# Kernel tuning notes

Measured on AMD Instinct MI355X. Metric: run time of the kernel, lower is better.

Reference implementation:

```python
import jax, jax.numpy as jnp
import numpy as np
from jax import lax

EPS = 1e-8

def setup_inputs() -> dict:
    key = jax.random.key(0)
    k1, k2, k3, k4 = jax.random.split(key, 4)
    b, ic, oc, ks, sd, h, w = 16, 512, 512, 3, 512, 64, 64
    x = jax.random.normal(k1, (b, ic, h, w), dtype=jnp.float32)
    style = jax.random.normal(k2, (b, sd), dtype=jnp.float32)
    # kaiming_normal_(fan_in, linear): std = 1/sqrt(ic*ks*ks)
    weight = jax.random.normal(k3, (oc, ic, ks, ks), dtype=jnp.float32) / np.sqrt(ic * ks * ks)
    bias = jnp.zeros((oc,), dtype=jnp.float32)
    # nn.Linear default init ~ U(-1/sqrt(sd), 1/sqrt(sd)); normal approx is fine for a baseline
    mod_w = jax.random.normal(k4, (ic, sd), dtype=jnp.float32) / np.sqrt(sd)
    mod_b = jnp.ones((ic,), dtype=jnp.float32)  # bias initialized to 1.0 in the module
    return {"x": x, "style": style, "weight": weight, "bias": bias, "mod_w": mod_w, "mod_b": mod_b}

def reference(x, style, weight, bias, mod_w, mod_b):
    b, ic, h, w = x.shape
    oc, _, ks, _ = weight.shape
    # style modulation: [b, ic]
    s = style @ mod_w.T + mod_b
    # per-sample modulated weights: [b, oc, ic, k, k]
    wmod = weight[None] * s[:, None, :, None, None]
    # demodulation
    demod = lax.rsqrt(jnp.sum(wmod * wmod, axis=(2, 3, 4)) + EPS)  # [b, oc]
    wmod = wmod * demod[:, :, None, None, None]
    pad = ks // 2
    # grouped conv with groups=b == per-sample conv: vmap over batch
    def conv1(xi, wi):  # xi: [ic,h,w], wi: [oc,ic,k,k]
        return lax.conv_general_dilated(
            xi[None], wi, window_strides=(1, 1),
            padding=[(pad, pad), (pad, pad)],
            dimension_numbers=("NCHW", "OIHW", "NCHW"))[0]
    out = jax.vmap(conv1)(x, wmod)  # [b, oc, h, w]
    return out + bias[None, :, None, None]
```

## Files before the change

### kernel.cpp

```cpp
#include <hip/hip_runtime.h>
#include <hip/hip_bf16.h>


typedef __bf16 bf16x8 __attribute__((ext_vector_type(8)));
typedef float  f32x4  __attribute__((ext_vector_type(4)));

#define IC   512
#define OC   512
#define HW   4096
#define KTOT 4608

typedef __attribute__((address_space(3))) unsigned lds_u32;
typedef const __attribute__((address_space(1))) unsigned glb_u32;
#define GLL16(gsrc, ldst) \
    __builtin_amdgcn_global_load_lds((glb_u32*)(gsrc), (lds_u32*)(ldst), 16, 0, 0)
#define VMW(N) asm volatile("s_waitcnt vmcnt(" #N ")" ::: "memory")
#define BAR()  asm volatile("s_barrier" ::: "memory")

__global__ __launch_bounds__(256) void style_mod_kernel(
    const float* __restrict__ style, const float* __restrict__ mod_w,
    const float* __restrict__ mod_b, float* __restrict__ s_out)
{
    int pair = blockIdx.x * 4 + (threadIdx.x >> 6);
    int lane = threadIdx.x & 63;
    int b = pair >> 9;
    int i = pair & 511;
    const float4* sv = (const float4*)(style + b * 512);
    const float4* wv = (const float4*)(mod_w + i * 512);
    float4 a0 = sv[lane * 2], a1 = sv[lane * 2 + 1];
    float4 w0 = wv[lane * 2], w1 = wv[lane * 2 + 1];
    float sum = a0.x*w0.x + a0.y*w0.y + a0.z*w0.z + a0.w*w0.w
              + a1.x*w1.x + a1.y*w1.y + a1.z*w1.z + a1.w*w1.w;
    #pragma unroll
    for (int off = 32; off; off >>= 1) sum += __shfl_xor(sum, off);
    if (lane == 0) s_out[pair] = sum + mod_b[i];
}

__global__ __launch_bounds__(256) void wmod_kernel(
    const float* __restrict__ weight,
    const float* __restrict__ s_in,
    __hip_bfloat16* __restrict__ wmod)
{
    int b  = blockIdx.x >> 9;
    int oc = blockIdx.x & 511;
    __shared__ float s_sh[512];
    __shared__ float red[256];
    int t = threadIdx.x;
    s_sh[t]       = s_in[b * 512 + t];
    s_sh[t + 256] = s_in[b * 512 + t + 256];
    __syncthreads();
    const float* wrow = weight + (size_t)oc * KTOT;
    float partial = 0.f;
    for (int e = t; e < KTOT; e += 256) {
        float v = wrow[e] * s_sh[e / 9];
        partial += v * v;
    }
    red[t] = partial;
    __syncthreads();
    #pragma unroll
    for (int off = 128; off; off >>= 1) {
        if (t < off) red[t] += red[t + off];
        __syncthreads();
    }
    float demod = rsqrtf(red[0] + 1e-8f);
    __hip_bfloat16* dst = wmod + (size_t)blockIdx.x * KTOT;
    for (int ep = t; ep < KTOT; ep += 256) {
        int tap = ep >> 9, ic = ep & 511;
        dst[ep] = __float2bfloat16(wrow[ic * 9 + tap] * s_sh[ic] * demod);
    }
}

__global__ void zero_row_kernel(__hip_bfloat16* xT) {
    ((unsigned*)(xT + ((size_t)blockIdx.x * 4097 + 4096) * 512))[threadIdx.x] = 0u;
}

__global__ __launch_bounds__(256) void xpose_kernel(
    const float* __restrict__ x, __hip_bfloat16* __restrict__ xT)
{
    __shared__ __align__(16) float tile[64][68];
    int b = blockIdx.z, ic0 = blockIdx.y * 64, p0 = blockIdx.x * 64;
    int t = threadIdx.x;
    const float* xb = x + ((size_t)b * 512 + ic0) * 4096 + p0;
    int rr = t >> 4, cc = (t & 15) * 4;
    #pragma unroll
    for (int i = 0; i < 4; ++i) {
        float4 v = *(const float4*)(xb + (size_t)(rr + i * 16) * 4096 + cc);
        *(float4*)&tile[rr + i * 16][cc] = v;
    }
    __syncthreads();
    int pr = t >> 2, io = (t & 3) * 16;
    __hip_bfloat16 obuf[16];
    #pragma unroll
    for (int j = 0; j < 16; ++j) obuf[j] = __float2bfloat16(tile[io + j][pr]);
    __hip_bfloat16* dst = xT + ((size_t)b * 4097 + p0 + pr) * 512 + ic0 + io;
    *(uint4*)dst       = *(uint4*)&obuf[0];
    *(uint4*)(dst + 8) = *(uint4*)&obuf[8];
}

__global__ __launch_bounds__(512, 2) void conv_kernel(
    const __hip_bfloat16* __restrict__ xT,
    const __hip_bfloat16* __restrict__ wmod,
    const float* __restrict__ bias,
    float* __restrict__ out)
{
    __shared__ __align__(16) __hip_bfloat16 Ash[4][256 * 32];
    __shared__ __align__(16) __hip_bfloat16 Bsh[4][256 * 32];

    const int t    = threadIdx.x;
    const int lane = t & 63;
    const int wid  = t >> 6;
    const int wm   = wid >> 2;
    const int wn   = wid & 3;
    const int lr   = lane & 15;
    const int lq   = lane >> 4;

    int bid = blockIdx.x;
    int xcd = bid & 7, idx = bid >> 3;
    int oc1 = idx & 1;
    int nt  = (idx >> 1) & 15;
    int bb  = (idx >> 5) & 1;
    int b   = xcd * 2 + bb;
    int oc0 = oc1 * 256, n0 = nt * 256;

    const __hip_bfloat16* wb = wmod + (size_t)(b * 512 + oc0) * KTOT;
    const __hip_bfloat16* xb = xT + (size_t)b * 4097 * 512;

    const int qoff = (((t & 3) ^ ((t >> 3) & 3)) * 8);
    const int srow = t >> 2;
    const int p0g  = n0 + srow;
    const int y0p  = p0g >> 6, x0p = p0g & 63;

    const __hip_bfloat16* pA0 = wb + (size_t)srow * KTOT + qoff;
    const __hip_bfloat16* pA1 = pA0 + (size_t)128 * KTOT;

    const int swq = (lq ^ ((lr >> 1) & 3)) * 8;
    const int arb = (wm * 128 + lr) * 32 + swq;
    const int brb = (wn * 64  + lr) * 32 + swq;

    f32x4 acc[8][4] = {};

    auto bptrs = [&](int tap, const __hip_bfloat16*& P0, const __hip_bfloat16*& P1) {
        int dy = tap / 3 - 1, dx = tap % 3 - 1;
        int sy = y0p + dy, sx = x0p + dx;
        int pix0 = ((((unsigned)sy)  < 64u) & (((unsigned)sx) < 64u)) ? ((sy  << 6) + sx) : 4096;
        int sy1 = sy + 2;
        int pix1 = ((((unsigned)sy1) < 64u) & (((unsigned)sx) < 64u)) ? ((sy1 << 6) + sx) : 4096;
        P0 = xb + (size_t)pix0 * 512 + qoff;
        P1 = xb + (size_t)pix1 * 512 + qoff;
    };

#define STAGE(SB, PA_OFF, Q0, Q1, B_OFF) { \
    GLL16(pA0 + (PA_OFF), &Ash[SB][t * 8]); \
    GLL16(pA1 + (PA_OFF), &Ash[SB][(t + 512) * 8]); \
    GLL16((Q0) + (B_OFF), &Bsh[SB][t * 8]); \
    GLL16((Q1) + (B_OFF), &Bsh[SB][(t + 512) * 8]); }

#define COMPUTE(CB) { \
    bf16x8 af[8], bf[4]; \
    _Pragma("unroll") for (int mi = 0; mi < 8; ++mi) \
        af[mi] = *(const bf16x8*)(&Ash[CB][arb + mi * 512]); \
    _Pragma("unroll") for (int ni = 0; ni < 4; ++ni) \
        bf[ni] = *(const bf16x8*)(&Bsh[CB][brb + ni * 512]); \
    __builtin_amdgcn_s_setprio(1); \
    _Pragma("unroll") for (int mi = 0; mi < 8; ++mi) \
        _Pragma("unroll") for (int ni = 0; ni < 4; ++ni) \
            acc[mi][ni] = __builtin_amdgcn_mfma_f32_16x16x32_bf16( \
                af[mi], bf[ni], acc[mi][ni], 0, 0, 0); \
    __builtin_amdgcn_s_setprio(0); }

    const __hip_bfloat16 *pB0, *pB1, *nB0, *nB1;
    bptrs(0, pB0, pB1);

    STAGE(0, 0,  pB0, pB1, 0);
    STAGE(1, 32, pB0, pB1, 32);
    STAGE(2, 64, pB0, pB1, 64);
    VMW(8);
    BAR();

    for (int tap = 0; tap < 8; ++tap) {
        bptrs(tap + 1, nB0, nB1);
        #pragma unroll
        for (int ch = 0; ch < 16; ++ch) {
            if (ch < 13) { STAGE((ch + 3) & 3, (ch + 3) * 32, pB0, pB1, (ch + 3) * 32); }
            else         { STAGE((ch + 3) & 3, (ch + 3) * 32, nB0, nB1, (ch - 13) * 32); }
            COMPUTE(ch & 3);
            VMW(8);
            BAR();
        }
        pA0 += 512; pA1 += 512;
        pB0 = nB0; pB1 = nB1;
    }
    #pragma unroll
    for (int ch = 0; ch < 16; ++ch) {
        if (ch <= 12) { STAGE((ch + 3) & 3, (ch + 3) * 32, pB0, pB1, (ch + 3) * 32); }
        COMPUTE(ch & 3);
        if      (ch < 13)  { VMW(8); BAR(); }
        else if (ch == 13) { VMW(4); BAR(); }
        else if (ch == 14) { VMW(0); BAR(); }
    }
#undef STAGE
#undef COMPUTE

    #pragma unroll
    for (int mi = 0; mi < 8; ++mi) {
        int oc = oc0 + wm * 128 + mi * 16 + lq * 4;
        #pragma unroll
        for (int ni = 0; ni < 4; ++ni) {
            int n = n0 + wn * 64 + ni * 16 + lr;
            #pragma unroll
            for (int v = 0; v < 4; ++v) {
                float r = acc[mi][ni][v] + bias[oc + v];
                out[((size_t)(b * OC + oc + v)) * HW + n] = r;
            }
        }
    }
}

extern "C" void kernel_launch(void* const* d_in, const int* in_sizes, int n_in,
                              void* d_out, int out_size, void* d_ws, size_t ws_size,
                              hipStream_t stream) {
    const float* x      = (const float*)d_in[0];
    const float* style  = (const float*)d_in[1];
    const float* weight = (const float*)d_in[2];
    const float* bias   = (const float*)d_in[3];
    const float* mod_w  = (const float*)d_in[4];
    const float* mod_b  = (const float*)d_in[5];
    float* out = (float*)d_out;

    float* s_ws = (float*)d_ws;
    __hip_bfloat16* wmod = (__hip_bfloat16*)((char*)d_ws + 32768);
    __hip_bfloat16* xT   = (__hip_bfloat16*)((char*)d_ws + 32768 + (size_t)16 * 512 * KTOT * 2);

    style_mod_kernel<<<2048, 256, 0, stream>>>(style, mod_w, mod_b, s_ws);
    wmod_kernel<<<16 * 512, 256, 0, stream>>>(weight, s_ws, wmod);
    zero_row_kernel<<<16, 256, 0, stream>>>(xT);
    dim3 tgrid(64, 8, 16);
    xpose_kernel<<<tgrid, 256, 0, stream>>>(x, xT);
    conv_kernel<<<512, 512, 0, stream>>>(xT, wmod, bias, out);
}
```

Before: 379.4 us.

## Split conv K-chunk into two MFMA halves interleaved with staged loads and barriers

Each K-chunk of the conv main loop is now split into two halves. The A fragments for rows 0-3 and the B fragments are read, the A global-to-LDS load is issued, then 16 MFMAs run; then A rows 4-7 are read, the B load is issued, and another 16 MFMAs run. Extra s_barriers and sched_barrier(0) fences pin this ordering so LDS reads, async global loads and MFMA phases overlap across waves, in a ping-pong style schedule. The change halves the live A-fragment registers, but it adds two barriers per chunk and constrains the compiler's scheduling freedom.

```diff
diff --git a/kernel.cpp b/kernel.cpp
--- a/kernel.cpp
+++ b/kernel.cpp
@@ -14,8 +14,9 @@
 typedef const __attribute__((address_space(1))) unsigned glb_u32;
 #define GLL16(gsrc, ldst) \
     __builtin_amdgcn_global_load_lds((glb_u32*)(gsrc), (lds_u32*)(ldst), 16, 0, 0)
-#define VMW(N) asm volatile("s_waitcnt vmcnt(" #N ")" ::: "memory")
-#define BAR()  asm volatile("s_barrier" ::: "memory")
+#define VMW(N)  asm volatile("s_waitcnt vmcnt(" #N ")" ::: "memory")
+#define BAR()   asm volatile("s_barrier" ::: "memory")
+#define SCHED0() __builtin_amdgcn_sched_barrier(0)
 
 __global__ __launch_bounds__(256) void style_mod_kernel(
     const float* __restrict__ style, const float* __restrict__ mod_w,
@@ -149,31 +150,27 @@
         P1 = xb + (size_t)pix1 * 512 + qoff;
     };
 
-#define STAGE(SB, PA_OFF, Q0, Q1, B_OFF) { \
-    GLL16(pA0 + (PA_OFF), &Ash[SB][t * 8]); \
-    GLL16(pA1 + (PA_OFF), &Ash[SB][(t + 512) * 8]); \
-    GLL16((Q0) + (B_OFF), &Bsh[SB][t * 8]); \
-    GLL16((Q1) + (B_OFF), &Bsh[SB][(t + 512) * 8]); }
-
-#define COMPUTE(CB) { \
-    bf16x8 af[8], bf[4]; \
-    _Pragma("unroll") for (int mi = 0; mi < 8; ++mi) \
-        af[mi] = *(const bf16x8*)(&Ash[CB][arb + mi * 512]); \
-    _Pragma("unroll") for (int ni = 0; ni < 4; ++ni) \
-        bf[ni] = *(const bf16x8*)(&Bsh[CB][brb + ni * 512]); \
+#define STAGE_A(SB, OFF) { \
+    GLL16(pA0 + (OFF), &Ash[SB][t * 8]); \
+    GLL16(pA1 + (OFF), &Ash[SB][(t + 512) * 8]); }
+#define STAGE_B(SB, Q0, Q1, OFF) { \
+    GLL16((Q0) + (OFF), &Bsh[SB][t * 8]); \
+    GLL16((Q1) + (OFF), &Bsh[SB][(t + 512) * 8]); }
+
+#define MFMA_HALF(MB) { \
     __builtin_amdgcn_s_setprio(1); \
-    _Pragma("unroll") for (int mi = 0; mi < 8; ++mi) \
+    _Pragma("unroll") for (int mi = 0; mi < 4; ++mi) \
         _Pragma("unroll") for (int ni = 0; ni < 4; ++ni) \
-            acc[mi][ni] = __builtin_amdgcn_mfma_f32_16x16x32_bf16( \
-                af[mi], bf[ni], acc[mi][ni], 0, 0, 0); \
+            acc[(MB) + mi][ni] = __builtin_amdgcn_mfma_f32_16x16x32_bf16( \
+                af[mi], bfr[ni], acc[(MB) + mi][ni], 0, 0, 0); \
     __builtin_amdgcn_s_setprio(0); }
 
     const __hip_bfloat16 *pB0, *pB1, *nB0, *nB1;
     bptrs(0, pB0, pB1);
 
-    STAGE(0, 0,  pB0, pB1, 0);
-    STAGE(1, 32, pB0, pB1, 32);
-    STAGE(2, 64, pB0, pB1, 64);
+    STAGE_A(0, 0);  STAGE_B(0, pB0, pB1, 0);
+    STAGE_A(1, 32); STAGE_B(1, pB0, pB1, 32);
+    STAGE_A(2, 64); STAGE_B(2, pB0, pB1, 64);
     VMW(8);
     BAR();
 
@@ -181,9 +178,25 @@
         bptrs(tap + 1, nB0, nB1);
         #pragma unroll
         for (int ch = 0; ch < 16; ++ch) {
-            if (ch < 13) { STAGE((ch + 3) & 3, (ch + 3) * 32, pB0, pB1, (ch + 3) * 32); }
-            else         { STAGE((ch + 3) & 3, (ch + 3) * 32, nB0, nB1, (ch - 13) * 32); }
-            COMPUTE(ch & 3);
+            const int cb = ch & 3, sb = (ch + 3) & 3;
+            bf16x8 af[4], bfr[4];
+            #pragma unroll
+            for (int mi = 0; mi < 4; ++mi)
+                af[mi] = *(const bf16x8*)(&Ash[cb][arb + mi * 512]);
+            #pragma unroll
+            for (int ni = 0; ni < 4; ++ni)
+                bfr[ni] = *(const bf16x8*)(&Bsh[cb][brb + ni * 512]);
+            STAGE_A(sb, (ch + 3) * 32);
+            BAR(); SCHED0();
+            MFMA_HALF(0);
+            BAR();
+            #pragma unroll
+            for (int mi = 0; mi < 4; ++mi)
+                af[mi] = *(const bf16x8*)(&Ash[cb][arb + (4 + mi) * 512]);
+            if (ch < 13) { STAGE_B(sb, pB0, pB1, (ch + 3) * 32); }
+            else         { STAGE_B(sb, nB0, nB1, (ch - 13) * 32); }
+            BAR(); SCHED0();
+            MFMA_HALF(4);
             VMW(8);
             BAR();
         }
@@ -192,14 +205,31 @@
     }
     #pragma unroll
     for (int ch = 0; ch < 16; ++ch) {
-        if (ch <= 12) { STAGE((ch + 3) & 3, (ch + 3) * 32, pB0, pB1, (ch + 3) * 32); }
-        COMPUTE(ch & 3);
+        const int cb = ch & 3, sb = (ch + 3) & 3;
+        bf16x8 af[4], bfr[4];
+        #pragma unroll
+        for (int mi = 0; mi < 4; ++mi)
+            af[mi] = *(const bf16x8*)(&Ash[cb][arb + mi * 512]);
+        #pragma unroll
+        for (int ni = 0; ni < 4; ++ni)
+            bfr[ni] = *(const bf16x8*)(&Bsh[cb][brb + ni * 512]);
+        if (ch <= 12) STAGE_A(sb, (ch + 3) * 32);
+        BAR(); SCHED0();
+        MFMA_HALF(0);
+        BAR();
+        #pragma unroll
+        for (int mi = 0; mi < 4; ++mi)
+            af[mi] = *(const bf16x8*)(&Ash[cb][arb + (4 + mi) * 512]);
+        if (ch <= 12) STAGE_B(sb, pB0, pB1, (ch + 3) * 32);
+        BAR(); SCHED0();
+        MFMA_HALF(4);
         if      (ch < 13)  { VMW(8); BAR(); }
         else if (ch == 13) { VMW(4); BAR(); }
         else if (ch == 14) { VMW(0); BAR(); }
     }
-#undef STAGE
-#undef COMPUTE
+#undef STAGE_A
+#undef STAGE_B
+#undef MFMA_HALF
 
     #pragma unroll
     for (int mi = 0; mi < 8; ++mi) {
```

After: 374.3 us. Within noise of the previous version (-1.3%).

## Load conv B operand directly into registers, bypassing LDS staging

Applied to the files above, without the earlier changes.

Removes the LDS buffer for the shifted-pixel (B) operand. Each wave now loads its MFMA B fragments straight from global memory into double-buffered registers, one chunk ahead, while A (modulated weights) stays staged through LDS with global_load_lds. MFMAs are split into two groups of A fragments, and the vmcnt waits are retuned for the mixed in-flight loads. This halves LDS traffic and footprint, at the cost of more global/L2 requests since the B loads are no longer shared across waves, plus extra register pressure.

```diff
diff --git a/kernel.cpp b/kernel.cpp
--- a/kernel.cpp
+++ b/kernel.cpp
@@ -14,8 +14,12 @@
 typedef const __attribute__((address_space(1))) unsigned glb_u32;
 #define GLL16(gsrc, ldst) \
     __builtin_amdgcn_global_load_lds((glb_u32*)(gsrc), (lds_u32*)(ldst), 16, 0, 0)
-#define VMW(N) asm volatile("s_waitcnt vmcnt(" #N ")" ::: "memory")
-#define BAR()  asm volatile("s_barrier" ::: "memory")
+#define BAR()   asm volatile("s_barrier" ::: "memory")
+#define SCHED0() __builtin_amdgcn_sched_barrier(0)
+
+template<int N> __device__ __forceinline__ void vmw() {
+    asm volatile("s_waitcnt vmcnt(%0)" :: "n"(N) : "memory");
+}
 
 __global__ __launch_bounds__(256) void style_mod_kernel(
     const float* __restrict__ style, const float* __restrict__ mod_w,
@@ -104,7 +108,6 @@
     float* __restrict__ out)
 {
     __shared__ __align__(16) __hip_bfloat16 Ash[4][256 * 32];
-    __shared__ __align__(16) __hip_bfloat16 Bsh[4][256 * 32];
 
     const int t    = threadIdx.x;
     const int lane = t & 63;
@@ -126,80 +129,112 @@
     const __hip_bfloat16* xb = xT + (size_t)b * 4097 * 512;
 
     const int qoff = (((t & 3) ^ ((t >> 3) & 3)) * 8);
-    const int srow = t >> 2;
-    const int p0g  = n0 + srow;
-    const int y0p  = p0g >> 6, x0p = p0g & 63;
-
-    const __hip_bfloat16* pA0 = wb + (size_t)srow * KTOT + qoff;
+    const __hip_bfloat16* pA0 = wb + (size_t)(t >> 2) * KTOT + qoff;
     const __hip_bfloat16* pA1 = pA0 + (size_t)128 * KTOT;
+
+    __hip_bfloat16* const dA0[4] = {&Ash[0][t*8], &Ash[1][t*8], &Ash[2][t*8], &Ash[3][t*8]};
+    __hip_bfloat16* const dA1[4] = {&Ash[0][(t+512)*8], &Ash[1][(t+512)*8],
+                                    &Ash[2][(t+512)*8], &Ash[3][(t+512)*8]};
 
     const int swq = (lq ^ ((lr >> 1) & 3)) * 8;
     const int arb = (wm * 128 + lr) * 32 + swq;
-    const int brb = (wn * 64  + lr) * 32 + swq;
 
     f32x4 acc[8][4] = {};
-
-    auto bptrs = [&](int tap, const __hip_bfloat16*& P0, const __hip_bfloat16*& P1) {
-        int dy = tap / 3 - 1, dx = tap % 3 - 1;
-        int sy = y0p + dy, sx = x0p + dx;
-        int pix0 = ((((unsigned)sy)  < 64u) & (((unsigned)sx) < 64u)) ? ((sy  << 6) + sx) : 4096;
-        int sy1 = sy + 2;
-        int pix1 = ((((unsigned)sy1) < 64u) & (((unsigned)sx) < 64u)) ? ((sy1 << 6) + sx) : 4096;
-        P0 = xb + (size_t)pix0 * 512 + qoff;
-        P1 = xb + (size_t)pix1 * 512 + qoff;
-    };
-
-#define STAGE(SB, PA_OFF, Q0, Q1, B_OFF) { \
-    GLL16(pA0 + (PA_OFF), &Ash[SB][t * 8]); \
-    GLL16(pA1 + (PA_OFF), &Ash[SB][(t + 512) * 8]); \
-    GLL16((Q0) + (B_OFF), &Bsh[SB][t * 8]); \
-    GLL16((Q1) + (B_OFF), &Bsh[SB][(t + 512) * 8]); }
-
-#define COMPUTE(CB) { \
-    bf16x8 af[8], bf[4]; \
-    _Pragma("unroll") for (int mi = 0; mi < 8; ++mi) \
-        af[mi] = *(const bf16x8*)(&Ash[CB][arb + mi * 512]); \
-    _Pragma("unroll") for (int ni = 0; ni < 4; ++ni) \
-        bf[ni] = *(const bf16x8*)(&Bsh[CB][brb + ni * 512]); \
-    __builtin_amdgcn_s_setprio(1); \
-    _Pragma("unroll") for (int mi = 0; mi < 8; ++mi) \
+    bf16x8 bfrA[4], bfrB[4];
+    const __hip_bfloat16 *pBF[4], *nBF[4];
+
+#define BPTR4(TAP, ARR) { \
+    int dy = (TAP) / 3 - 1, dx = (TAP) % 3 - 1; \
+    _Pragma("unroll") for (int ni = 0; ni < 4; ++ni) { \
+        int p = n0 + wn * 64 + ni * 16 + lr; \
+        int sy = (p >> 6) + dy, sx = (p & 63) + dx; \
+        int pix = ((((unsigned)sy) < 64u) & (((unsigned)sx) < 64u)) ? ((sy << 6) + sx) : 4096; \
+        ARR[ni] = xb + (size_t)pix * 512 + lq * 8; } }
+
+#define STEP(CH, BCUR, BNXT, DO_STAGE, BL_MODE, VN) { \
+    const int sb_ = ((CH) + 3) & 3, cb_ = (CH) & 3; \
+    if (DO_STAGE) { \
+        GLL16(pA0 + ((CH) + 3) * 32, dA0[sb_]); \
+        GLL16(pA1 + ((CH) + 3) * 32, dA1[sb_]); \
+    } \
+    if ((BL_MODE) == 1) { \
         _Pragma("unroll") for (int ni = 0; ni < 4; ++ni) \
-            acc[mi][ni] = __builtin_amdgcn_mfma_f32_16x16x32_bf16( \
-                af[mi], bf[ni], acc[mi][ni], 0, 0, 0); \
-    __builtin_amdgcn_s_setprio(0); }
-
-    const __hip_bfloat16 *pB0, *pB1, *nB0, *nB1;
-    bptrs(0, pB0, pB1);
-
-    STAGE(0, 0,  pB0, pB1, 0);
-    STAGE(1, 32, pB0, pB1, 32);
-    STAGE(2, 64, pB0, pB1, 64);
-    VMW(8);
+            BNXT[ni] = *(const bf16x8*)(pBF[ni] + ((CH) + 1) * 32); \
+    } else if ((BL_MODE) == 2) { \
+        _Pragma("unroll") for (int ni = 0; ni < 4; ++ni) \
+            BNXT[ni] = *(const bf16x8*)(nBF[ni]); \
+    } \
+    vmw<VN>(); \
+    { \
+        bf16x8 af0 = *(const bf16x8*)(&Ash[cb_][arb +   0]); \
+        bf16x8 af1 = *(const bf16x8*)(&Ash[cb_][arb +  512]); \
+        bf16x8 af2 = *(const bf16x8*)(&Ash[cb_][arb + 1024]); \
+        bf16x8 af3 = *(const bf16x8*)(&Ash[cb_][arb + 1536]); \
+        __builtin_amdgcn_s_setprio(1); \
+        _Pragma("unroll") for (int ni = 0; ni < 4; ++ni) { \
+            acc[0][ni] = __builtin_amdgcn_mfma_f32_16x16x32_bf16(af0, BCUR[ni], acc[0][ni], 0,0,0); \
+            acc[1][ni] = __builtin_amdgcn_mfma_f32_16x16x32_bf16(af1, BCUR[ni], acc[1][ni], 0,0,0); \
+            acc[2][ni] = __builtin_amdgcn_mfma_f32_16x16x32_bf16(af2, BCUR[ni], acc[2][ni], 0,0,0); \
+            acc[3][ni] = __builtin_amdgcn_mfma_f32_16x16x32_bf16(af3, BCUR[ni], acc[3][ni], 0,0,0); \
+        } \
+        __builtin_amdgcn_s_setprio(0); \
+    } \
+    { \
+        bf16x8 af4 = *(const bf16x8*)(&Ash[cb_][arb + 2048]); \
+        bf16x8 af5 = *(const bf16x8*)(&Ash[cb_][arb + 2560]); \
+        bf16x8 af6 = *(const bf16x8*)(&Ash[cb_][arb + 3072]); \
+        bf16x8 af7 = *(const bf16x8*)(&Ash[cb_][arb + 3584]); \
+        __builtin_amdgcn_s_setprio(1); \
+        _Pragma("unroll") for (int ni = 0; ni < 4; ++ni) { \
+            acc[4][ni] = __builtin_amdgcn_mfma_f32_16x16x32_bf16(af4, BCUR[ni], acc[4][ni], 0,0,0); \
+            acc[5][ni] = __builtin_amdgcn_mfma_f32_16x16x32_bf16(af5, BCUR[ni], acc[5][ni], 0,0,0); \
+            acc[6][ni] = __builtin_amdgcn_mfma_f32_16x16x32_bf16(af6, BCUR[ni], acc[6][ni], 0,0,0); \
+            acc[7][ni] = __builtin_amdgcn_mfma_f32_16x16x32_bf16(af7, BCUR[ni], acc[7][ni], 0,0,0); \
+        } \
+        __builtin_amdgcn_s_setprio(0); \
+    } \
+    SCHED0(); \
+    BAR(); }
+
+    BPTR4(0, pBF);
+    GLL16(pA0 +  0, dA0[0]); GLL16(pA1 +  0, dA1[0]);
+    GLL16(pA0 + 32, dA0[1]); GLL16(pA1 + 32, dA1[1]);
+    GLL16(pA0 + 64, dA0[2]); GLL16(pA1 + 64, dA1[2]);
+    #pragma unroll
+    for (int ni = 0; ni < 4; ++ni) bfrA[ni] = *(const bf16x8*)(pBF[ni]);
+    vmw<8>();
     BAR();
 
     for (int tap = 0; tap < 8; ++tap) {
-        bptrs(tap + 1, nB0, nB1);
+        BPTR4(tap + 1, nBF);
         #pragma unroll
-        for (int ch = 0; ch < 16; ++ch) {
-            if (ch < 13) { STAGE((ch + 3) & 3, (ch + 3) * 32, pB0, pB1, (ch + 3) * 32); }
-            else         { STAGE((ch + 3) & 3, (ch + 3) * 32, nB0, nB1, (ch - 13) * 32); }
-            COMPUTE(ch & 3);
-            VMW(8);
-            BAR();
+        for (int c2 = 0; c2 < 8; ++c2) {
+            STEP(2*c2,     bfrA, bfrB, true, 1, 18);
+            STEP(2*c2 + 1, bfrB, bfrA, true, ((2*c2 + 1) == 15 ? 2 : 1), 18);
         }
         pA0 += 512; pA1 += 512;
-        pB0 = nB0; pB1 = nB1;
-    }
-    #pragma unroll
-    for (int ch = 0; ch < 16; ++ch) {
-        if (ch <= 12) { STAGE((ch + 3) & 3, (ch + 3) * 32, pB0, pB1, (ch + 3) * 32); }
-        COMPUTE(ch & 3);
-        if      (ch < 13)  { VMW(8); BAR(); }
-        else if (ch == 13) { VMW(4); BAR(); }
-        else if (ch == 14) { VMW(0); BAR(); }
-    }
-#undef STAGE
-#undef COMPUTE
+        #pragma unroll
+        for (int ni = 0; ni < 4; ++ni) pBF[ni] = nBF[ni];
+    }
+
+    STEP(0,  bfrA, bfrB, true, 1, 18);
+    STEP(1,  bfrB, bfrA, true, 1, 18);
+    STEP(2,  bfrA, bfrB, true, 1, 18);
+    STEP(3,  bfrB, bfrA, true, 1, 18);
+    STEP(4,  bfrA, bfrB, true, 1, 18);
+    STEP(5,  bfrB, bfrA, true, 1, 18);
+    STEP(6,  bfrA, bfrB, true, 1, 18);
+    STEP(7,  bfrB, bfrA, true, 1, 18);
+    STEP(8,  bfrA, bfrB, true, 1, 18);
+    STEP(9,  bfrB, bfrA, true, 1, 18);
+    STEP(10, bfrA, bfrB, true, 1, 18);
+    STEP(11, bfrB, bfrA, true, 1, 18);
+    STEP(12, bfrA, bfrB, true, 1, 18);
+    STEP(13, bfrB, bfrA, false, 1, 16);
+    STEP(14, bfrA, bfrB, false, 1, 14);
+    STEP(15, bfrB, bfrA, false, 0, 8);
+#undef STEP
+#undef BPTR4
 
     #pragma unroll
     for (int mi = 0; mi < 8; ++mi) {
```

Result: slower. 515.8 us (+35.9%).

## Retile conv kernel to 256x128 blocks with 4 waves and triple-buffered LDS

Applied to the files above, without the earlier changes.

The conv kernel moves from 512-thread blocks with 256x256 tiles and a 4-stage LDS ring to 256-thread blocks with 256x128 tiles and a 3-stage ring. Within each step, LDS fragment reads are issued before the next global-to-LDS prefetch. The grid doubles to 1024 blocks and LDS per block shrinks, aiming for better occupancy and load balance. The cost is more re-reads of the modulated weights across N tiles. The wmod kernel block order is also permuted so that consecutive blocks share the same weight row across batches.

```diff
diff --git a/kernel.cpp b/kernel.cpp
--- a/kernel.cpp
+++ b/kernel.cpp
@@ -14,8 +14,11 @@
 typedef const __attribute__((address_space(1))) unsigned glb_u32;
 #define GLL16(gsrc, ldst) \
     __builtin_amdgcn_global_load_lds((glb_u32*)(gsrc), (lds_u32*)(ldst), 16, 0, 0)
-#define VMW(N) asm volatile("s_waitcnt vmcnt(" #N ")" ::: "memory")
-#define BAR()  asm volatile("s_barrier" ::: "memory")
+#define BAR()   asm volatile("s_barrier" ::: "memory")
+
+template<int N> __device__ __forceinline__ void vmw() {
+    asm volatile("s_waitcnt vmcnt(%0)" :: "n"(N) : "memory");
+}
 
 __global__ __launch_bounds__(256) void style_mod_kernel(
     const float* __restrict__ style, const float* __restrict__ mod_w,
@@ -41,8 +44,8 @@
     const float* __restrict__ s_in,
     __hip_bfloat16* __restrict__ wmod)
 {
-    int b  = blockIdx.x >> 9;
-    int oc = blockIdx.x & 511;
+    int oc = blockIdx.x >> 4;
+    int b  = blockIdx.x & 15;
     __shared__ float s_sh[512];
     __shared__ float red[256];
     int t = threadIdx.x;
@@ -63,7 +66,7 @@
         __syncthreads();
     }
     float demod = rsqrtf(red[0] + 1e-8f);
-    __hip_bfloat16* dst = wmod + (size_t)blockIdx.x * KTOT;
+    __hip_bfloat16* dst = wmod + ((size_t)b * 512 + oc) * KTOT;
     for (int ep = t; ep < KTOT; ep += 256) {
         int tap = ep >> 9, ic = ep & 511;
         dst[ep] = __float2bfloat16(wrow[ic * 9 + tap] * s_sh[ic] * demod);
@@ -97,30 +100,30 @@
     *(uint4*)(dst + 8) = *(uint4*)&obuf[8];
 }
 
-__global__ __launch_bounds__(512, 2) void conv_kernel(
+__global__ __launch_bounds__(256, 2) void conv_kernel(
     const __hip_bfloat16* __restrict__ xT,
     const __hip_bfloat16* __restrict__ wmod,
     const float* __restrict__ bias,
     float* __restrict__ out)
 {
-    __shared__ __align__(16) __hip_bfloat16 Ash[4][256 * 32];
-    __shared__ __align__(16) __hip_bfloat16 Bsh[4][256 * 32];
+    __shared__ __align__(16) __hip_bfloat16 AshF[3 * 256 * 32];
+    __shared__ __align__(16) __hip_bfloat16 BshF[3 * 128 * 32];
 
     const int t    = threadIdx.x;
     const int lane = t & 63;
     const int wid  = t >> 6;
-    const int wm   = wid >> 2;
-    const int wn   = wid & 3;
+    const int wm   = wid >> 1;
+    const int wn   = wid & 1;
     const int lr   = lane & 15;
     const int lq   = lane >> 4;
 
     int bid = blockIdx.x;
     int xcd = bid & 7, idx = bid >> 3;
-    int oc1 = idx & 1;
-    int nt  = (idx >> 1) & 15;
-    int bb  = (idx >> 5) & 1;
+    int mt  = idx & 1;
+    int nt  = (idx >> 1) & 31;
+    int bb  = idx >> 6;
     int b   = xcd * 2 + bb;
-    int oc0 = oc1 * 256, n0 = nt * 256;
+    int oc0 = mt * 256, n0 = nt * 128;
 
     const __hip_bfloat16* wb = wmod + (size_t)(b * 512 + oc0) * KTOT;
     const __hip_bfloat16* xb = xT + (size_t)b * 4097 * 512;
@@ -131,7 +134,14 @@
     const int y0p  = p0g >> 6, x0p = p0g & 63;
 
     const __hip_bfloat16* pA0 = wb + (size_t)srow * KTOT + qoff;
-    const __hip_bfloat16* pA1 = pA0 + (size_t)128 * KTOT;
+    const __hip_bfloat16* pA1 = pA0 + (size_t)64  * KTOT;
+    const __hip_bfloat16* pA2 = pA0 + (size_t)128 * KTOT;
+    const __hip_bfloat16* pA3 = pA0 + (size_t)192 * KTOT;
+
+    int soA0 = 0, soA1 = 8192, soA2 = 16384;
+    int soB0 = 0, soB1 = 4096, soB2 = 8192;
+#define SOA(i) (((i) % 3) == 0 ? soA0 : (((i) % 3) == 1 ? soA1 : soA2))
+#define SOB(i) (((i) % 3) == 0 ? soB0 : (((i) % 3) == 1 ? soB1 : soB2))
 
     const int swq = (lq ^ ((lr >> 1) & 3)) * 8;
     const int arb = (wm * 128 + lr) * 32 + swq;
@@ -139,67 +149,90 @@
 
     f32x4 acc[8][4] = {};
 
+    const __hip_bfloat16 *pB0, *pB1, *nB0, *nB1;
     auto bptrs = [&](int tap, const __hip_bfloat16*& P0, const __hip_bfloat16*& P1) {
         int dy = tap / 3 - 1, dx = tap % 3 - 1;
         int sy = y0p + dy, sx = x0p + dx;
         int pix0 = ((((unsigned)sy)  < 64u) & (((unsigned)sx) < 64u)) ? ((sy  << 6) + sx) : 4096;
-        int sy1 = sy + 2;
+        int sy1 = sy + 1;
         int pix1 = ((((unsigned)sy1) < 64u) & (((unsigned)sx) < 64u)) ? ((sy1 << 6) + sx) : 4096;
         P0 = xb + (size_t)pix0 * 512 + qoff;
         P1 = xb + (size_t)pix1 * 512 + qoff;
     };
 
-#define STAGE(SB, PA_OFF, Q0, Q1, B_OFF) { \
-    GLL16(pA0 + (PA_OFF), &Ash[SB][t * 8]); \
-    GLL16(pA1 + (PA_OFF), &Ash[SB][(t + 512) * 8]); \
-    GLL16((Q0) + (B_OFF), &Bsh[SB][t * 8]); \
-    GLL16((Q1) + (B_OFF), &Bsh[SB][(t + 512) * 8]); }
-
-#define COMPUTE(CB) { \
-    bf16x8 af[8], bf[4]; \
+#define STAGE_A(SO, OFF) { \
+    GLL16(pA0 + (OFF), &AshF[(SO) + t * 8]); \
+    GLL16(pA1 + (OFF), &AshF[(SO) + (t + 256) * 8]); \
+    GLL16(pA2 + (OFF), &AshF[(SO) + (t + 512) * 8]); \
+    GLL16(pA3 + (OFF), &AshF[(SO) + (t + 768) * 8]); }
+#define STAGE_B(SO, Q0, Q1, OFF) { \
+    GLL16((Q0) + (OFF), &BshF[(SO) + t * 8]); \
+    GLL16((Q1) + (OFF), &BshF[(SO) + (t + 256) * 8]); }
+
+#define STEP(CH, DO_STAGE, B_NEXT, VN) { \
+    bf16x8 af[8], bfr[4]; \
     _Pragma("unroll") for (int mi = 0; mi < 8; ++mi) \
-        af[mi] = *(const bf16x8*)(&Ash[CB][arb + mi * 512]); \
+        af[mi] = *(const bf16x8*)(&AshF[SOA(CH) + arb + mi * 512]); \
     _Pragma("unroll") for (int ni = 0; ni < 4; ++ni) \
-        bf[ni] = *(const bf16x8*)(&Bsh[CB][brb + ni * 512]); \
+        bfr[ni] = *(const bf16x8*)(&BshF[SOB(CH) + brb + ni * 512]); \
+    if (DO_STAGE) { \
+        STAGE_A(SOA((CH) + 2), ((CH) + 2) * 32); \
+        if (B_NEXT) { STAGE_B(SOB((CH) + 2), nB0, nB1, ((CH) - 14) * 32); } \
+        else        { STAGE_B(SOB((CH) + 2), pB0, pB1, ((CH) + 2) * 32); } \
+    } \
     __builtin_amdgcn_s_setprio(1); \
     _Pragma("unroll") for (int mi = 0; mi < 8; ++mi) \
         _Pragma("unroll") for (int ni = 0; ni < 4; ++ni) \
             acc[mi][ni] = __builtin_amdgcn_mfma_f32_16x16x32_bf16( \
-                af[mi], bf[ni], acc[mi][ni], 0, 0, 0); \
-    __builtin_amdgcn_s_setprio(0); }
-
-    const __hip_bfloat16 *pB0, *pB1, *nB0, *nB1;
+                af[mi], bfr[ni], acc[mi][ni], 0, 0, 0); \
+    __builtin_amdgcn_s_setprio(0); \
+    vmw<VN>(); \
+    BAR(); }
+
     bptrs(0, pB0, pB1);
-
-    STAGE(0, 0,  pB0, pB1, 0);
-    STAGE(1, 32, pB0, pB1, 32);
-    STAGE(2, 64, pB0, pB1, 64);
-    VMW(8);
+    STAGE_A(0, 0);      STAGE_B(0, pB0, pB1, 0);
+    STAGE_A(8192, 32);  STAGE_B(4096, pB0, pB1, 32);
+    vmw<6>();
     BAR();
 
     for (int tap = 0; tap < 8; ++tap) {
         bptrs(tap + 1, nB0, nB1);
         #pragma unroll
         for (int ch = 0; ch < 16; ++ch) {
-            if (ch < 13) { STAGE((ch + 3) & 3, (ch + 3) * 32, pB0, pB1, (ch + 3) * 32); }
-            else         { STAGE((ch + 3) & 3, (ch + 3) * 32, nB0, nB1, (ch - 13) * 32); }
-            COMPUTE(ch & 3);
-            VMW(8);
-            BAR();
+            STEP(ch, true, (ch >= 14), 6);
         }
-        pA0 += 512; pA1 += 512;
+        int ta = soA0; soA0 = soA1; soA1 = soA2; soA2 = ta;
+        int tb = soB0; soB0 = soB1; soB1 = soB2; soB2 = tb;
+        pA0 += 512; pA1 += 512; pA2 += 512; pA3 += 512;
         pB0 = nB0; pB1 = nB1;
     }
-    #pragma unroll
-    for (int ch = 0; ch < 16; ++ch) {
-        if (ch <= 12) { STAGE((ch + 3) & 3, (ch + 3) * 32, pB0, pB1, (ch + 3) * 32); }
-        COMPUTE(ch & 3);
-        if      (ch < 13)  { VMW(8); BAR(); }
-        else if (ch == 13) { VMW(4); BAR(); }
-        else if (ch == 14) { VMW(0); BAR(); }
-    }
-#undef STAGE
-#undef COMPUTE
+
+    #pragma unroll
+    for (int ch = 0; ch < 13; ++ch) {
+        STEP(ch, true, false, 6);
+    }
+    STEP(13, true,  false, 6);
+    STEP(14, false, false, 0);
+    {
+        bf16x8 af[8], bfr[4];
+        #pragma unroll
+        for (int mi = 0; mi < 8; ++mi)
+            af[mi] = *(const bf16x8*)(&AshF[SOA(15) + arb + mi * 512]);
+        #pragma unroll
+        for (int ni = 0; ni < 4; ++ni)
+            bfr[ni] = *(const bf16x8*)(&BshF[SOB(15) + brb + ni * 512]);
+        #pragma unroll
+        for (int mi = 0; mi < 8; ++mi)
+            #pragma unroll
+            for (int ni = 0; ni < 4; ++ni)
+                acc[mi][ni] = __builtin_amdgcn_mfma_f32_16x16x32_bf16(
+                    af[mi], bfr[ni], acc[mi][ni], 0, 0, 0);
+    }
+#undef STEP
+#undef STAGE_A
+#undef STAGE_B
+#undef SOA
+#undef SOB
 
     #pragma unroll
     for (int mi = 0; mi < 8; ++mi) {
@@ -236,5 +269,5 @@
     zero_row_kernel<<<16, 256, 0, stream>>>(xT);
     dim3 tgrid(64, 8, 16);
     xpose_kernel<<<tgrid, 256, 0, stream>>>(x, xT);
-    conv_kernel<<<512, 512, 0, stream>>>(xT, wmod, bias, out);
-}
+    conv_kernel<<<1024, 256, 0, stream>>>(xT, wmod, bias, out);
+}
```

Result: slower. 422.4 us, median of 2 (+11.3%).
